# Kernel tuning notes

Hardware: AMD Instinct MI355X
Metric: run time of the kernel (lower is better)

Reference implementation:

```python
import jax, jax.numpy as jnp
import numpy as np

N_NODES = 100000
N_EDGES = 3200000
N_FEAT = 512
N_HID = 256
N_CLASS = 40
K_HOPS = 10


def setup_inputs() -> dict:
    key = jax.random.key(0)
    ks = jax.random.split(key, 8)
    feature = jax.random.normal(ks[0], (N_NODES, N_FEAT), dtype=jnp.float32)
    edge_row = jax.random.randint(ks[1], (N_EDGES,), 0, N_NODES, dtype=jnp.int32)
    edge_col = jax.random.randint(ks[2], (N_EDGES,), 0, N_NODES, dtype=jnp.int32)
    edge_weight = jax.random.uniform(ks[3], (N_EDGES,), dtype=jnp.float32)
    W1 = jax.random.normal(ks[4], (N_FEAT, N_HID), dtype=jnp.float32) * (1.0 / np.sqrt(N_FEAT))
    b1 = jnp.zeros((N_HID,), dtype=jnp.float32)
    W2 = jax.random.normal(ks[5], (N_HID, N_CLASS), dtype=jnp.float32) * (1.0 / np.sqrt(N_HID))
    b2 = jnp.zeros((N_CLASS,), dtype=jnp.float32)
    Wa = jax.random.normal(ks[6], (N_CLASS, 1), dtype=jnp.float32) * (1.0 / np.sqrt(N_CLASS))
    ba = jnp.zeros((1,), dtype=jnp.float32)
    return {"feature": feature, "edge_row": edge_row, "edge_col": edge_col,
            "edge_weight": edge_weight, "W1": W1, "b1": b1, "W2": W2, "b2": b2,
            "Wa": Wa, "ba": ba}


def reference(feature, edge_row, edge_col, edge_weight, W1, b1, W2, b2, Wa, ba):
    # eval mode: dropout is identity
    x = jax.nn.relu(feature @ W1 + b1)          # [N, H]
    x = x @ W2 + b2                              # [N, C]
    # k-hop sparse propagation: out[i] = sum_e w_e * x[col_e] for row_e == i
    xs = [x]
    for _ in range(K_HOPS):
        x = jax.ops.segment_sum(edge_weight[:, None] * x[edge_col], edge_row,
                                num_segments=N_NODES)
        xs.append(x)
    xs = jnp.stack(xs, axis=1)                   # [N, K+1, C]
    score = jax.nn.sigmoid(jnp.squeeze(xs @ Wa + ba, -1))  # [N, K+1]
    out = jnp.einsum('nk,nkc->nc', score, xs)    # attention-weighted hop sum
    return jax.nn.log_softmax(out, axis=1)
```

## Files before the change

### kernel.cpp

```cpp
#include <hip/hip_runtime.h>
#include <math.h>

#define N_NODES 100000
#define N_EDGES 3200000
#define N_FEAT  512
#define N_HID   256
#define N_CLASS 40
#define K_HOPS  10

#define CAP        80

#define BIN_SHIFT  11
#define NBIN       49
#define NBIN_PAD   56
#define BINCAP     68000
#define CHUNK1     4096
#define CHUNK2     4096
#define CPB2       17

typedef __attribute__((ext_vector_type(8))) short short8;
typedef __attribute__((ext_vector_type(8))) unsigned short ushort8v;
typedef __attribute__((ext_vector_type(4))) float float4v;
typedef unsigned long long u64;

__device__ inline short f2bf(float f)
{
    union { float f; unsigned u; } v; v.f = f;
    unsigned r = v.u + 0x7FFF + ((v.u >> 16) & 1);
    return (short)(r >> 16);
}

__device__ inline float bf2f(unsigned short u)
{
    union { unsigned u; float f; } v; v.u = (unsigned)u << 16;
    return v.f;
}

__global__ void pack_w1(const float* __restrict__ W1, short* __restrict__ W1p)
{
    const int id = blockIdx.x * 256 + threadIdx.x;
    const int kb = id >> 8, n = id & 255;
    short tmp[32];
#pragma unroll
    for (int kl = 0; kl < 32; ++kl)
        tmp[kl] = f2bf(W1[(size_t)(kb * 32 + kl) * N_HID + n]);
    short8* dst = (short8*)&W1p[id * 32];
#pragma unroll
    for (int j = 0; j < 4; ++j) dst[j] = *(short8*)&tmp[j * 8];
}

__global__ void pack_w2(const float* __restrict__ W2, short* __restrict__ W2p)
{
    const int id = blockIdx.x * 256 + threadIdx.x;
    if (id >= 8 * 48) return;
    const int kb = id / 48, n = id % 48;
    short tmp[32];
#pragma unroll
    for (int kl = 0; kl < 32; ++kl)
        tmp[kl] = (n < N_CLASS) ? f2bf(W2[(size_t)(kb * 32 + kl) * N_CLASS + n]) : (short)0;
    short8* dst = (short8*)&W2p[id * 32];
#pragma unroll
    for (int j = 0; j < 4; ++j) dst[j] = *(short8*)&tmp[j * 8];
}

__global__ __launch_bounds__(256) void mlp_mfma(
    const float* __restrict__ feat, const short* __restrict__ W1p,
    const float* __restrict__ b1, const short* __restrict__ W2p,
    const float* __restrict__ b2, const float* __restrict__ Wa,
    const float* __restrict__ ba,
    unsigned short* __restrict__ x0, float* __restrict__ acc_out)
{
    __shared__ __align__(16) short smem[64 * 264];
    short (*As)[40]  = (short(*)[40])smem;
    short (*Hs)[264] = (short(*)[264])smem;

    const int t    = threadIdx.x;
    const int wave = t >> 6;
    const int lane = t & 63;
    const int q    = lane >> 4;
    const int m    = lane & 15;
    const int n0   = blockIdx.x * 64;
    const int colbase = wave * 64;

    float4v acc[4][4];
#pragma unroll
    for (int i = 0; i < 4; ++i)
#pragma unroll
        for (int j = 0; j < 4; ++j) acc[i][j] = (float4v)0.f;

    for (int kb = 0; kb < 16; ++kb) {
        const int k0 = kb * 32;
        __syncthreads();
        {
            const int r  = t >> 2;
            const int kq = t & 3;
            const int n  = n0 + r;
            float f[8];
            if (n < N_NODES) {
                const float* p = &feat[(size_t)n * N_FEAT + k0 + 8 * kq];
                float4 v0 = *(const float4*)p;
                float4 v1 = *(const float4*)(p + 4);
                f[0]=v0.x; f[1]=v0.y; f[2]=v0.z; f[3]=v0.w;
                f[4]=v1.x; f[5]=v1.y; f[6]=v1.z; f[7]=v1.w;
            } else {
#pragma unroll
                for (int j = 0; j < 8; ++j) f[j] = 0.f;
            }
            short8 st;
#pragma unroll
            for (int j = 0; j < 8; ++j) st[j] = f2bf(f[j]);
            *(short8*)&As[r][8 * kq] = st;
        }
        __syncthreads();

        short8 af[4], bfr[4];
#pragma unroll
        for (int rt = 0; rt < 4; ++rt)
            af[rt] = *(const short8*)&As[rt * 16 + m][q * 8];
#pragma unroll
        for (int ct = 0; ct < 4; ++ct) {
            const int off = (kb * 256 + colbase + ct * 16 + m) * 32 + q * 8;
            bfr[ct] = *(const short8*)&W1p[off];
        }
#pragma unroll
        for (int rt = 0; rt < 4; ++rt)
#pragma unroll
            for (int ct = 0; ct < 4; ++ct)
                acc[rt][ct] = __builtin_amdgcn_mfma_f32_16x16x32_bf16(
                    af[rt], bfr[ct], acc[rt][ct], 0, 0, 0);
    }

    __syncthreads();
#pragma unroll
    for (int ct = 0; ct < 4; ++ct) {
        const int col = colbase + ct * 16 + m;
        const float bias = b1[col];
#pragma unroll
        for (int rt = 0; rt < 4; ++rt) {
            const float4v d = acc[rt][ct];
#pragma unroll
            for (int r = 0; r < 4; ++r) {
                const float hv = fmaxf(d[r] + bias, 0.f);
                Hs[rt * 16 + q * 4 + r][col] = f2bf(hv);
            }
        }
    }
    __syncthreads();

    float4v acc2[3];
#pragma unroll
    for (int ct = 0; ct < 3; ++ct) acc2[ct] = (float4v)0.f;
#pragma unroll
    for (int kb = 0; kb < 8; ++kb) {
        const short8 a2 = *(const short8*)&Hs[wave * 16 + m][kb * 32 + q * 8];
#pragma unroll
        for (int ct = 0; ct < 3; ++ct) {
            const int off = (kb * 48 + ct * 16 + m) * 32 + q * 8;
            const short8 b2f = *(const short8*)&W2p[off];
            acc2[ct] = __builtin_amdgcn_mfma_f32_16x16x32_bf16(a2, b2f, acc2[ct], 0, 0, 0);
        }
    }

    float val[3][4];
#pragma unroll
    for (int ct = 0; ct < 3; ++ct) {
        const int col = ct * 16 + m;
        const bool cok = col < N_CLASS;
        const float bias = cok ? b2[col] : 0.f;
#pragma unroll
        for (int r = 0; r < 4; ++r) val[ct][r] = acc2[ct][r] + bias;
        if (cok) {
#pragma unroll
            for (int r = 0; r < 4; ++r) {
                const int row = n0 + wave * 16 + q * 4 + r;
                if (row < N_NODES)
                    x0[(size_t)row * N_CLASS + col] = (unsigned short)f2bf(val[ct][r]);
            }
        }
    }
    float part[4];
#pragma unroll
    for (int r = 0; r < 4; ++r) {
        float p = 0.f;
#pragma unroll
        for (int ct = 0; ct < 3; ++ct) {
            const int col = ct * 16 + m;
            if (col < N_CLASS) p += val[ct][r] * Wa[col];
        }
        part[r] = p;
    }
#pragma unroll
    for (int o = 1; o <= 8; o <<= 1)
#pragma unroll
        for (int r = 0; r < 4; ++r) part[r] += __shfl_xor(part[r], o);
    const float bb = ba[0];
#pragma unroll
    for (int r = 0; r < 4; ++r) {
        const int row = n0 + wave * 16 + q * 4 + r;
        if (row < N_NODES) {
            const float sc = 1.f / (1.f + expf(-(part[r] + bb)));
#pragma unroll
            for (int ct = 0; ct < 3; ++ct) {
                const int col = ct * 16 + m;
                if (col < N_CLASS)
                    acc_out[(size_t)row * N_CLASS + col] = sc * val[ct][r];
            }
        }
    }
}

__global__ __launch_bounds__(256) void bin_kernel(
    const int* __restrict__ erow, const int* __restrict__ ecol,
    const float* __restrict__ ew, int* __restrict__ bin_cursor,
    u64* __restrict__ bins)
{
    __shared__ __align__(16) u64 recs[CHUNK1];
    __shared__ int hist[NBIN], h2[NBIN], lbase[NBIN], adj[NBIN];

    const int t     = threadIdx.x;
    const int cbase = blockIdx.x * CHUNK1;
    const int e0    = cbase + t * 16;
    const bool has  = e0 < N_EDGES;
    const int chunk_n = min(CHUNK1, N_EDGES - cbase);

    for (int i = t; i < NBIN; i += 256) { hist[i] = 0; h2[i] = 0; }
    __syncthreads();

    int   rows[16], cols[16], w15[16];
    if (has) {
#pragma unroll
        for (int qv = 0; qv < 4; ++qv) {
            const int4   r = *(const int4*)&erow[e0 + qv * 4];
            const int4   c = *(const int4*)&ecol[e0 + qv * 4];
            const float4 w = *(const float4*)&ew[e0 + qv * 4];
            rows[qv*4+0]=r.x; rows[qv*4+1]=r.y; rows[qv*4+2]=r.z; rows[qv*4+3]=r.w;
            cols[qv*4+0]=c.x; cols[qv*4+1]=c.y; cols[qv*4+2]=c.z; cols[qv*4+3]=c.w;
            const float wf[4] = {w.x, w.y, w.z, w.w};
#pragma unroll
            for (int j = 0; j < 4; ++j) {
                int v = (int)(wf[j] * 32767.f + 0.5f);
                w15[qv*4+j] = (v > 32767) ? 32767 : v;
            }
        }
#pragma unroll
        for (int j = 0; j < 16; ++j)
            atomicAdd(&hist[rows[j] >> BIN_SHIFT], 1);
    }
    __syncthreads();

    if (t == 0) {
        int run = 0;
        for (int b = 0; b < NBIN; ++b) { lbase[b] = run; run += hist[b]; }
    }
    __syncthreads();
    if (t < NBIN) {
        const int g = atomicAdd(&bin_cursor[t], hist[t]);
        adj[t] = g - lbase[t];
    }
    __syncthreads();

    if (has) {
#pragma unroll
        for (int j = 0; j < 16; ++j) {
            const int b = rows[j] >> BIN_SHIFT;
            const int p = lbase[b] + atomicAdd(&h2[b], 1);
            recs[p] = ((u64)w15[j] << 34) | ((u64)rows[j] << 17) | (u64)cols[j];
        }
    }
    __syncthreads();

    for (int i = t; i < chunk_n; i += 256) {
        const u64 r   = recs[i];
        const int row = (int)((r >> 17) & 0x1FFFF);
        const int b   = row >> BIN_SHIFT;
        const int di  = adj[b] + i;
        if (di < BINCAP)
            bins[(size_t)b * BINCAP + di] = r;
    }
}

__global__ __launch_bounds__(256) void scatter_bins(
    const int* __restrict__ bin_cursor, const u64* __restrict__ bins,
    int* __restrict__ cnt, unsigned int* __restrict__ ebuck)
{
    const int b = blockIdx.x % NBIN_PAD;
    if (b >= NBIN) return;
    const int chunk = blockIdx.x / NBIN_PAD;
    int n = bin_cursor[b];
    if (n > BINCAP) n = BINCAP;
    const int start = chunk * CHUNK2;
    if (start >= n) return;
    const u64* src = &bins[(size_t)b * BINCAP];

#pragma unroll
    for (int j = 0; j < 16; ++j) {
        const int idx = start + j * 256 + threadIdx.x;
        if (idx < n) {
            const u64 r   = src[idx];
            const int col = (int)(r & 0x1FFFF);
            const int row = (int)((r >> 17) & 0x1FFFF);
            const unsigned rec = ((unsigned)(r >> 34) << 17) | (unsigned)col;
            const int pos = atomicAdd(&cnt[row], 1);
            if (pos < CAP)
                ebuck[(size_t)row * CAP + pos] = rec;
        }
    }
}

__global__ __launch_bounds__(256) void hop_kernel(
    const int* __restrict__ cnt, const unsigned int* __restrict__ ebuck,
    const unsigned short* __restrict__ xin,
    unsigned short* __restrict__ xout, float* __restrict__ acc,
    const float* __restrict__ Wa, const float* __restrict__ ba)
{
    const int lane = threadIdx.x & 63;
    const int row  = blockIdx.x * 4 + (threadIdx.x >> 6);
    if (row >= N_NODES) return;
    const int  slot = lane >> 3;
    const int  l    = lane & 7;
    const bool act  = l < 5;

    int n = cnt[row];
    if (n > CAP) n = CAP;
    const size_t ebase = (size_t)row * CAP;

    unsigned rec_a = (lane < n) ? ebuck[ebase + lane] : 0u;

    float s[8];
#pragma unroll
    for (int j = 0; j < 8; ++j) s[j] = 0.f;

    const int nmain = (n < 64) ? n : 64;
    for (int e = 0; e < nmain; e += 8) {
        const unsigned r = __shfl(rec_a, e + slot);
        const int   col  = (int)(r & 0x1FFFFu);
        const float w    = (float)(r >> 17) * (1.f / 32767.f);
        if (act) {
            const ushort8v v = *(const ushort8v*)&xin[(size_t)col * N_CLASS + l * 8];
#pragma unroll
            for (int j = 0; j < 8; ++j) s[j] += w * bf2f(v[j]);
        }
    }
    for (int e = 64; e < n; e += 8) {
        const int ee = e + slot;
        unsigned r = 0u;
        if (ee < n) r = ebuck[ebase + ee];
        const int   col = (int)(r & 0x1FFFFu);
        const float w   = (float)(r >> 17) * (1.f / 32767.f);
        if (act) {
            const ushort8v v = *(const ushort8v*)&xin[(size_t)col * N_CLASS + l * 8];
#pragma unroll
            for (int j = 0; j < 8; ++j) s[j] += w * bf2f(v[j]);
        }
    }

#pragma unroll
    for (int o = 8; o <= 32; o <<= 1)
#pragma unroll
        for (int j = 0; j < 8; ++j) s[j] += __shfl_xor(s[j], o);

    float tq = 0.f;
    if (act) {
#pragma unroll
        for (int j = 0; j < 8; ++j) tq += s[j] * Wa[l * 8 + j];
    }
#pragma unroll
    for (int o = 1; o <= 4; o <<= 1) tq += __shfl_xor(tq, o);
    const float z  = tq + ba[0];
    const float sc = 1.f / (1.f + expf(-z));

    if (act && slot == 0) {
        ushort8v ov;
#pragma unroll
        for (int j = 0; j < 8; ++j) ov[j] = (unsigned short)f2bf(s[j]);
        *(ushort8v*)&xout[(size_t)row * N_CLASS + l * 8] = ov;

        float4* ap0 = (float4*)&acc[(size_t)row * N_CLASS + l * 8];
        float4 a0 = ap0[0];
        float4 a1 = ap0[1];
        a0.x += sc * s[0]; a0.y += sc * s[1]; a0.z += sc * s[2]; a0.w += sc * s[3];
        a1.x += sc * s[4]; a1.y += sc * s[5]; a1.z += sc * s[6]; a1.w += sc * s[7];
        ap0[0] = a0;
        ap0[1] = a1;
    }
}

__device__ inline float wave_sum(float v)
{
#pragma unroll
    for (int o = 32; o; o >>= 1) v += __shfl_xor(v, o);
    return v;
}

__global__ __launch_bounds__(256) void logsoftmax_kernel(
    const float* __restrict__ acc, float* __restrict__ out)
{
    const int lane = threadIdx.x & 63;
    const int row  = blockIdx.x * 4 + (threadIdx.x >> 6);
    if (row >= N_NODES) return;
    const int  c   = lane;
    const bool act = c < N_CLASS;

    float v = act ? acc[(size_t)row * N_CLASS + c] : -INFINITY;
    float mx = v;
#pragma unroll
    for (int o = 32; o; o >>= 1) mx = fmaxf(mx, __shfl_xor(mx, o));
    const float e = act ? expf(v - mx) : 0.f;
    const float s = wave_sum(e);
    if (act) out[(size_t)row * N_CLASS + c] = v - mx - logf(s);
}

extern "C" void kernel_launch(void* const* d_in, const int* in_sizes, int n_in,
                              void* d_out, int out_size, void* d_ws, size_t ws_size,
                              hipStream_t stream)
{
    (void)in_sizes; (void)n_in; (void)out_size; (void)ws_size;
    const float* feat = (const float*)d_in[0];
    const int*   erow = (const int*)d_in[1];
    const int*   ecol = (const int*)d_in[2];
    const float* ew   = (const float*)d_in[3];
    const float* W1   = (const float*)d_in[4];
    const float* b1   = (const float*)d_in[5];
    const float* W2   = (const float*)d_in[6];
    const float* b2   = (const float*)d_in[7];
    const float* Wa   = (const float*)d_in[8];
    const float* ba   = (const float*)d_in[9];
    float* out = (float*)d_out;

    char* ws = (char*)d_ws;
    size_t off = 0;
    auto take = [&](size_t bytes) -> char* {
        char* p = ws + off;
        off += (bytes + 255) & ~(size_t)255;
        return p;
    };
    unsigned short* xb0 = (unsigned short*)take((size_t)N_NODES * N_CLASS * 2 + 64);
    unsigned short* xb1 = (unsigned short*)take((size_t)N_NODES * N_CLASS * 2 + 64);
    float*        acc   = (float*)take((size_t)N_NODES * N_CLASS * 4);
    int*          cnt   = (int*)take((size_t)N_NODES * 4);
    int*          bcur  = (int*)take((size_t)NBIN_PAD * 4);
    short*        W1p   = (short*)take((size_t)N_FEAT * N_HID * 2);
    short*        W2p   = (short*)take((size_t)N_HID * 48 * 2);
    unsigned int* ebuck = (unsigned int*)take((size_t)N_NODES * CAP * 4);
    u64*          bins  = (u64*)take((size_t)NBIN * BINCAP * 8);

    hipMemsetAsync(cnt, 0, (size_t)N_NODES * 4, stream);
    hipMemsetAsync(bcur, 0, (size_t)NBIN_PAD * 4, stream);

    pack_w1<<<16, 256, 0, stream>>>(W1, W1p);
    pack_w2<<<2, 256, 0, stream>>>(W2, W2p);
    mlp_mfma<<<(N_NODES + 63) / 64, 256, 0, stream>>>(feat, W1p, b1, W2p, b2,
                                                      Wa, ba, xb0, acc);

    const int nchunk1 = (N_EDGES + CHUNK1 - 1) / CHUNK1;
    bin_kernel<<<nchunk1, 256, 0, stream>>>(erow, ecol, ew, bcur, bins);
    scatter_bins<<<NBIN_PAD * CPB2, 256, 0, stream>>>(bcur, bins, cnt, ebuck);

    const unsigned short* xin = xb0;
    unsigned short* xout = xb1;
    for (int k = 0; k < K_HOPS; ++k) {
        hop_kernel<<<N_NODES / 4, 256, 0, stream>>>(cnt, ebuck, xin, xout, acc, Wa, ba);
        unsigned short* tmp = (unsigned short*)xin;
        xin  = xout;
        xout = tmp;
    }

    logsoftmax_kernel<<<N_NODES / 4, 256, 0, stream>>>(acc, out);
}
```

Measured before the change: 1.174 ms.

## Stream features directly into MFMA registers and fuse log-softmax into last hop

```diff
diff --git a/kernel.cpp b/kernel.cpp
--- a/kernel.cpp
+++ b/kernel.cpp
@@ -36,6 +36,16 @@
     return v.f;
 }
 
+__device__ inline short8 cvt8(const float4& a, const float4& b)
+{
+    union { unsigned u[4]; short8 s; } r;
+    asm("v_cvt_pk_bf16_f32 %0, %1, %2" : "=v"(r.u[0]) : "v"(a.x), "v"(a.y));
+    asm("v_cvt_pk_bf16_f32 %0, %1, %2" : "=v"(r.u[1]) : "v"(a.z), "v"(a.w));
+    asm("v_cvt_pk_bf16_f32 %0, %1, %2" : "=v"(r.u[2]) : "v"(b.x), "v"(b.y));
+    asm("v_cvt_pk_bf16_f32 %0, %1, %2" : "=v"(r.u[3]) : "v"(b.z), "v"(b.w));
+    return r.s;
+}
+
 __global__ void pack_w1(const float* __restrict__ W1, short* __restrict__ W1p)
 {
     const int id = blockIdx.x * 256 + threadIdx.x;
@@ -63,7 +73,7 @@
     for (int j = 0; j < 4; ++j) dst[j] = *(short8*)&tmp[j * 8];
 }
 
-__global__ __launch_bounds__(256) void mlp_mfma(
+__global__ __launch_bounds__(256, 2) void mlp_mfma(
     const float* __restrict__ feat, const short* __restrict__ W1p,
     const float* __restrict__ b1, const short* __restrict__ W2p,
     const float* __restrict__ b2, const float* __restrict__ Wa,
@@ -71,7 +81,6 @@
     unsigned short* __restrict__ x0, float* __restrict__ acc_out)
 {
     __shared__ __align__(16) short smem[64 * 264];
-    short (*As)[40]  = (short(*)[40])smem;
     short (*Hs)[264] = (short(*)[264])smem;
 
     const int t    = threadIdx.x;
@@ -80,71 +89,80 @@
     const int q    = lane >> 4;
     const int m    = lane & 15;
     const int n0   = blockIdx.x * 64;
-    const int colbase = wave * 64;
-
-    float4v acc[4][4];
-#pragma unroll
-    for (int i = 0; i < 4; ++i)
-#pragma unroll
-        for (int j = 0; j < 4; ++j) acc[i][j] = (float4v)0.f;
-
+    const int RB   = wave >> 1;
+    const int CB   = wave & 1;
+
+    const float* ap[2];
+#pragma unroll
+    for (int rt = 0; rt < 2; ++rt) {
+        int r = n0 + RB * 32 + rt * 16 + m;
+        if (r > N_NODES - 1) r = N_NODES - 1;
+        ap[rt] = &feat[(size_t)r * N_FEAT + q * 8];
+    }
+    const short* bp = &W1p[(CB * 128 + m) * 32 + q * 8];
+
+    float4v acc[2][8];
+#pragma unroll
+    for (int rt = 0; rt < 2; ++rt)
+#pragma unroll
+        for (int ct = 0; ct < 8; ++ct) acc[rt][ct] = (float4v)0.f;
+
+    float4 A0[3][2], A1[3][2];
+    short8 Bp[2][8];
+
+#pragma unroll
+    for (int s = 0; s < 2; ++s)
+#pragma unroll
+        for (int rt = 0; rt < 2; ++rt) {
+            A0[s][rt] = *(const float4*)(ap[rt] + s * 32);
+            A1[s][rt] = *(const float4*)(ap[rt] + s * 32 + 4);
+        }
+#pragma unroll
+    for (int ct = 0; ct < 8; ++ct)
+        Bp[0][ct] = *(const short8*)(bp + (ct * 16) * 32);
+
+#pragma unroll
     for (int kb = 0; kb < 16; ++kb) {
-        const int k0 = kb * 32;
-        __syncthreads();
-        {
-            const int r  = t >> 2;
-            const int kq = t & 3;
-            const int n  = n0 + r;
-            float f[8];
-            if (n < N_NODES) {
-                const float* p = &feat[(size_t)n * N_FEAT + k0 + 8 * kq];
-                float4 v0 = *(const float4*)p;
-                float4 v1 = *(const float4*)(p + 4);
-                f[0]=v0.x; f[1]=v0.y; f[2]=v0.z; f[3]=v0.w;
-                f[4]=v1.x; f[5]=v1.y; f[6]=v1.z; f[7]=v1.w;
-            } else {
-#pragma unroll
-                for (int j = 0; j < 8; ++j) f[j] = 0.f;
+        const int sA_ld = (kb + 2) % 3;
+        const int sB_ld = (kb + 1) & 1;
+        const int sA    = kb % 3;
+        const int sB    = kb & 1;
+        if (kb + 2 < 16) {
+#pragma unroll
+            for (int rt = 0; rt < 2; ++rt) {
+                A0[sA_ld][rt] = *(const float4*)(ap[rt] + (kb + 2) * 32);
+                A1[sA_ld][rt] = *(const float4*)(ap[rt] + (kb + 2) * 32 + 4);
             }
-            short8 st;
-#pragma unroll
-            for (int j = 0; j < 8; ++j) st[j] = f2bf(f[j]);
-            *(short8*)&As[r][8 * kq] = st;
-        }
-        __syncthreads();
-
-        short8 af[4], bfr[4];
-#pragma unroll
-        for (int rt = 0; rt < 4; ++rt)
-            af[rt] = *(const short8*)&As[rt * 16 + m][q * 8];
-#pragma unroll
-        for (int ct = 0; ct < 4; ++ct) {
-            const int off = (kb * 256 + colbase + ct * 16 + m) * 32 + q * 8;
-            bfr[ct] = *(const short8*)&W1p[off];
-        }
-#pragma unroll
-        for (int rt = 0; rt < 4; ++rt)
-#pragma unroll
-            for (int ct = 0; ct < 4; ++ct)
+        }
+        if (kb + 1 < 16) {
+#pragma unroll
+            for (int ct = 0; ct < 8; ++ct)
+                Bp[sB_ld][ct] = *(const short8*)(bp + ((kb + 1) * 256 + ct * 16) * 32);
+        }
+        short8 a8[2];
+#pragma unroll
+        for (int rt = 0; rt < 2; ++rt) a8[rt] = cvt8(A0[sA][rt], A1[sA][rt]);
+#pragma unroll
+        for (int rt = 0; rt < 2; ++rt)
+#pragma unroll
+            for (int ct = 0; ct < 8; ++ct)
                 acc[rt][ct] = __builtin_amdgcn_mfma_f32_16x16x32_bf16(
-                    af[rt], bfr[ct], acc[rt][ct], 0, 0, 0);
-    }
-
-    __syncthreads();
-#pragma unroll
-    for (int ct = 0; ct < 4; ++ct) {
-        const int col = colbase + ct * 16 + m;
-        const float bias = b1[col];
-#pragma unroll
-        for (int rt = 0; rt < 4; ++rt) {
+                    a8[rt], Bp[sB][ct], acc[rt][ct], 0, 0, 0);
+    }
+
+#pragma unroll
+    for (int rt = 0; rt < 2; ++rt)
+#pragma unroll
+        for (int ct = 0; ct < 8; ++ct) {
+            const int col = CB * 128 + ct * 16 + m;
+            const float bias = b1[col];
             const float4v d = acc[rt][ct];
 #pragma unroll
             for (int r = 0; r < 4; ++r) {
-                const float hv = fmaxf(d[r] + bias, 0.f);
-                Hs[rt * 16 + q * 4 + r][col] = f2bf(hv);
+                const int row = RB * 32 + rt * 16 + q * 4 + r;
+                Hs[row][col] = f2bf(fmaxf(d[r] + bias, 0.f));
             }
         }
-    }
     __syncthreads();
 
     float4v acc2[3];
@@ -307,11 +325,13 @@
     }
 }
 
+template <bool LAST>
 __global__ __launch_bounds__(256) void hop_kernel(
     const int* __restrict__ cnt, const unsigned int* __restrict__ ebuck,
     const unsigned short* __restrict__ xin,
     unsigned short* __restrict__ xout, float* __restrict__ acc,
-    const float* __restrict__ Wa, const float* __restrict__ ba)
+    const float* __restrict__ Wa, const float* __restrict__ ba,
+    float* __restrict__ out)
 {
     const int lane = threadIdx.x & 63;
     const int row  = blockIdx.x * 4 + (threadIdx.x >> 6);
@@ -369,45 +389,58 @@
     const float z  = tq + ba[0];
     const float sc = 1.f / (1.f + expf(-z));
 
-    if (act && slot == 0) {
-        ushort8v ov;
-#pragma unroll
-        for (int j = 0; j < 8; ++j) ov[j] = (unsigned short)f2bf(s[j]);
-        *(ushort8v*)&xout[(size_t)row * N_CLASS + l * 8] = ov;
-
-        float4* ap0 = (float4*)&acc[(size_t)row * N_CLASS + l * 8];
-        float4 a0 = ap0[0];
-        float4 a1 = ap0[1];
-        a0.x += sc * s[0]; a0.y += sc * s[1]; a0.z += sc * s[2]; a0.w += sc * s[3];
-        a1.x += sc * s[4]; a1.y += sc * s[5]; a1.z += sc * s[6]; a1.w += sc * s[7];
-        ap0[0] = a0;
-        ap0[1] = a1;
-    }
-}
-
-__device__ inline float wave_sum(float v)
-{
-#pragma unroll
-    for (int o = 32; o; o >>= 1) v += __shfl_xor(v, o);
-    return v;
-}
-
-__global__ __launch_bounds__(256) void logsoftmax_kernel(
-    const float* __restrict__ acc, float* __restrict__ out)
-{
-    const int lane = threadIdx.x & 63;
-    const int row  = blockIdx.x * 4 + (threadIdx.x >> 6);
-    if (row >= N_NODES) return;
-    const int  c   = lane;
-    const bool act = c < N_CLASS;
-
-    float v = act ? acc[(size_t)row * N_CLASS + c] : -INFINITY;
-    float mx = v;
-#pragma unroll
-    for (int o = 32; o; o >>= 1) mx = fmaxf(mx, __shfl_xor(mx, o));
-    const float e = act ? expf(v - mx) : 0.f;
-    const float s = wave_sum(e);
-    if (act) out[(size_t)row * N_CLASS + c] = v - mx - logf(s);
+    const bool wr = act && slot == 0;
+    if (!LAST) {
+        if (wr) {
+            ushort8v ov;
+#pragma unroll
+            for (int j = 0; j < 8; ++j) ov[j] = (unsigned short)f2bf(s[j]);
+            *(ushort8v*)&xout[(size_t)row * N_CLASS + l * 8] = ov;
+
+            float4* ap0 = (float4*)&acc[(size_t)row * N_CLASS + l * 8];
+            float4 a0 = ap0[0];
+            float4 a1 = ap0[1];
+            a0.x += sc * s[0]; a0.y += sc * s[1]; a0.z += sc * s[2]; a0.w += sc * s[3];
+            a1.x += sc * s[4]; a1.y += sc * s[5]; a1.z += sc * s[6]; a1.w += sc * s[7];
+            ap0[0] = a0;
+            ap0[1] = a1;
+        }
+    } else {
+        float av[8];
+        float mxl = -INFINITY;
+        if (wr) {
+            const float4* ap0 = (const float4*)&acc[(size_t)row * N_CLASS + l * 8];
+            const float4 a0 = ap0[0];
+            const float4 a1 = ap0[1];
+            av[0] = a0.x + sc * s[0]; av[1] = a0.y + sc * s[1];
+            av[2] = a0.z + sc * s[2]; av[3] = a0.w + sc * s[3];
+            av[4] = a1.x + sc * s[4]; av[5] = a1.y + sc * s[5];
+            av[6] = a1.z + sc * s[6]; av[7] = a1.w + sc * s[7];
+#pragma unroll
+            for (int j = 0; j < 8; ++j) mxl = fmaxf(mxl, av[j]);
+        }
+        float mx = mxl;
+#pragma unroll
+        for (int o = 1; o <= 4; o <<= 1) mx = fmaxf(mx, __shfl_xor(mx, o));
+        float se = 0.f;
+        if (wr) {
+#pragma unroll
+            for (int j = 0; j < 8; ++j) se += expf(av[j] - mx);
+        }
+#pragma unroll
+        for (int o = 1; o <= 4; o <<= 1) se += __shfl_xor(se, o);
+        if (wr) {
+            const float ls = logf(se);
+            float4 o0, o1;
+            o0.x = av[0] - mx - ls; o0.y = av[1] - mx - ls;
+            o0.z = av[2] - mx - ls; o0.w = av[3] - mx - ls;
+            o1.x = av[4] - mx - ls; o1.y = av[5] - mx - ls;
+            o1.z = av[6] - mx - ls; o1.w = av[7] - mx - ls;
+            float4* op = (float4*)&out[(size_t)row * N_CLASS + l * 8];
+            op[0] = o0;
+            op[1] = o1;
+        }
+    }
 }
 
 extern "C" void kernel_launch(void* const* d_in, const int* in_sizes, int n_in,
@@ -458,12 +491,13 @@
 
     const unsigned short* xin = xb0;
     unsigned short* xout = xb1;
-    for (int k = 0; k < K_HOPS; ++k) {
-        hop_kernel<<<N_NODES / 4, 256, 0, stream>>>(cnt, ebuck, xin, xout, acc, Wa, ba);
+    for (int k = 0; k < K_HOPS - 1; ++k) {
+        hop_kernel<false><<<N_NODES / 4, 256, 0, stream>>>(
+            cnt, ebuck, xin, xout, acc, Wa, ba, out);
         unsigned short* tmp = (unsigned short*)xin;
         xin  = xout;
         xout = tmp;
     }
-
-    logsoftmax_kernel<<<N_NODES / 4, 256, 0, stream>>>(acc, out);
-}
+    hop_kernel<true><<<N_NODES / 4, 256, 0, stream>>>(
+        cnt, ebuck, xin, xout, acc, Wa, ba, out);
+}
```

Measured after the change: 1.200 ms. +2.2%, slower.
